# Optimization experiments

Measured on AMD Instinct MI355X. Metric: run time of the kernel, lower is better.

## Reference

```python
import jax, jax.numpy as jnp
import numpy as np

B, C, E, H = 8, 2048, 256, 64
N_AGENTS = 4
KAPPA = 0.9
MASKED = True


def _decay_xi_delta(dones):
    """Vectorized equivalent of get_decay_matrix / get_xi / delta.

    dones: [B, C] bool. Timestep dones are dones[:, ::N_AGENTS] -> [B, T].
    The original Python loop builds mask[b,n,m] = exists i with ts_done[b,i]
    and n >= i and m < i, i.e. a done strictly after m and at-or-before n.
    That equals (inclusive_cumsum[n] - inclusive_cumsum[m]) > 0.
    """
    ts = dones[:, ::N_AGENTS]                      # [B, T]
    T = ts.shape[1]
    csum = jnp.cumsum(ts.astype(jnp.int32), axis=1)            # inclusive
    blocked = (csum[:, :, None] - csum[:, None, :]) > 0        # [B, T, T]
    ts_mask = (~blocked).astype(jnp.float32)

    n = jnp.arange(T)
    diff = n[:, None] - n[None, :]
    dm = jnp.where(diff >= 0, KAPPA ** diff.astype(jnp.float32), 0.0)  # [T, T]
    dm = dm[None, :, :] * ts_mask                               # [B, T, T]
    # repeat_interleave over both time axes -> per-agent [B, C, C]
    dm = jnp.repeat(jnp.repeat(dm, N_AGENTS, axis=1), N_AGENTS, axis=2)
    if MASKED:
        Cfull = dm.shape[-1]
        dm = dm * jnp.tril(jnp.ones((Cfull, Cfull), dm.dtype))[None]

    # xi: kappa^(t+1) before the first done, 0 after (per timestep, repeated per agent)
    has_done = jnp.any(ts, axis=1, keepdims=True)               # [B, 1]
    first = jnp.argmax(ts.astype(jnp.float32), axis=1, keepdims=True)
    first = jnp.where(has_done, first, T)                       # [B, 1]
    t_idx = jnp.arange(T)[None, :]                              # [1, T]
    xi = (KAPPA ** (t_idx + 1).astype(jnp.float32)) * (t_idx < first).astype(jnp.float32)
    xi = jnp.repeat(xi, N_AGENTS, axis=1)[:, :, None]           # [B, C, 1]

    delta = (~jnp.any(ts, axis=1)).astype(jnp.float32)[:, None, None]  # [B,1,1]
    return dm, xi, delta


def setup_inputs() -> dict:
    key = jax.random.key(0)
    ks = jax.random.split(key, 8)
    return {
        "key_in": jax.random.normal(ks[0], (B, C, E), jnp.float32),
        "query": jax.random.normal(ks[1], (B, C, E), jnp.float32),
        "value": jax.random.normal(ks[2], (B, C, E), jnp.float32),
        "hstate": jax.random.normal(ks[3], (B, H, H), jnp.float32),
        "dones": jax.random.randint(ks[4], (B, C), 0, 2).astype(bool),
        "w_q": jax.random.normal(ks[5], (E, H), jnp.float32) / np.sqrt(E).astype(np.float32),
        "w_k": jax.random.normal(ks[6], (E, H), jnp.float32) / np.sqrt(E).astype(np.float32),
        "w_v": jax.random.normal(ks[7], (E, H), jnp.float32) / np.sqrt(E).astype(np.float32),
    }


def reference(key_in, query, value, hstate, dones, w_q, w_k, w_v):
    q = query @ w_q                                  # [B, C, H]
    k = key_in @ w_k                                 # [B, C, H]
    v = value @ w_v                                  # [B, C, H]

    dm, xi, delta = _decay_xi_delta(dones)           # [B,C,C], [B,C,1], [B,1,1]
    T = C // N_AGENTS
    chunk_decay = KAPPA ** T

    # next_hstate = k^T @ (v * last_row_of_decay^T) + hstate * chunk_decay * delta
    next_h = jnp.einsum('bch,bcd->bhd', k, v * dm[:, -1, :, None]) \
        + hstate * chunk_decay * delta

    cross = jnp.einsum('bch,bhd->bcd', q, hstate) * xi         # [B, C, H]
    scores = jnp.einsum('bch,bmh->bcm', q, k) * dm              # [B, C, C]
    inner = jnp.einsum('bcm,bmd->bcd', scores, v)               # [B, C, H]
    return inner + cross, next_h
```

## Files before the change

kernel.cpp:

```cpp
#include <hip/hip_runtime.h>
#include <hip/hip_bf16.h>
#include <cstddef>

#define B_ 8
#define C_ 2048
#define E_ 256
#define H_ 64
#define T_ 512
#define NA 4
#define KAPPA 0.9f
#define LOG2_KAPPA (-0.15200309344504997f)
#define KAPPA_T 3.73302e-24f

typedef __attribute__((ext_vector_type(8))) short bf16x8;
typedef __attribute__((ext_vector_type(4))) float f32x4;
typedef __attribute__((ext_vector_type(4))) unsigned u32x4;

__device__ inline unsigned short f2bfu(float x) {
    unsigned u = __builtin_bit_cast(unsigned, x);
    u += 0x7fff + ((u >> 16) & 1);
    return (unsigned short)(u >> 16);
}
__device__ inline float bf2f(unsigned short u) {
    return __builtin_bit_cast(float, (unsigned)u << 16);
}
__device__ inline unsigned pack2bf(float lo, float hi) {
    return (unsigned)f2bfu(lo) | ((unsigned)f2bfu(hi) << 16);
}
__device__ inline unsigned cvtpk(float a, float b) {
    __hip_bfloat162 h = __float22bfloat162_rn(float2{a, b});
    unsigned r;
    __builtin_memcpy(&r, &h, sizeof(r));
    return r;
}

__global__ __launch_bounds__(256) void proj_mfma(
    const float* __restrict__ key_in, const float* __restrict__ query,
    const float* __restrict__ value,
    const float* __restrict__ w_q, const float* __restrict__ w_k,
    const float* __restrict__ w_v,
    const unsigned char* __restrict__ raw,
    unsigned short* __restrict__ qp, unsigned short* __restrict__ kp,
    unsigned short* __restrict__ vp, int* __restrict__ s_tab)
{
    __shared__ __align__(16) char Wt[64 * 512];
    const int t   = threadIdx.x;
    const int bid = blockIdx.x;

    if (bid >= 768) {
        const int b    = bid - 768;
        const int lane = t & 63;
        const int w    = t >> 6;
        __shared__ int f;
        __shared__ unsigned long long msk[8];
        if (t == 0) f = 0;
        __syncthreads();
        {
            const uint4* dp = (const uint4*)raw;
            unsigned acc = 0;
#pragma unroll
            for (int i = 0; i < 4; ++i) {
                uint4 v = dp[t + 256 * i];
                acc |= (v.x | v.y | v.z | v.w) & 0xFFFFFF00u;
            }
            if (acc) f = 1;
        }
        __syncthreads();
        const int stride = f ? 1 : 4;
        const unsigned char* drow = raw + (size_t)b * C_ * stride;
#pragma unroll
        for (int cc = 0; cc < 2; ++cc) {
            const int c = 2 * w + cc;
            const int n = c * 64 + lane;
            unsigned long long m = __ballot(drow[(size_t)(4 * n) * stride] != 0);
            if (lane == 0) msk[c] = m;
        }
        __syncthreads();
#pragma unroll
        for (int cc = 0; cc < 2; ++cc) {
            const int c = 2 * w + cc;
            const int n = c * 64 + lane;
            unsigned long long lowmask =
                (lane == 63) ? ~0ULL : ((1ULL << (lane + 1)) - 1ULL);
            unsigned long long m_le = msk[c] & lowmask;
            int s = -1;
            if (m_le) {
                s = c * 64 + (63 - __builtin_clzll(m_le));
            } else {
                for (int c2 = c - 1; c2 >= 0; --c2)
                    if (msk[c2]) { s = c2 * 64 + (63 - __builtin_clzll(msk[c2])); break; }
            }
            s_tab[b * T_ + n] = s;
        }
        return;
    }

    const int mat = bid >> 8;
    const float* A; unsigned short* O16; const float* Wg;
    if (mat == 0)      { A = query;  O16 = qp; Wg = w_q; }
    else if (mat == 1) { A = key_in; O16 = kp; Wg = w_k; }
    else               { A = value;  O16 = vp; Wg = w_v; }

    const int b    = bid & 7;
    const int rb   = (bid & 255) >> 3;
    const int row0 = b * C_ + rb * 64;
    const int lane = t & 63;
    const int mt   = t >> 6;
    const int lr   = lane & 15;
    const int lg   = lane >> 4;
    const int swz  = (lr & 7) << 4;

#pragma unroll
    for (int p = 0; p < 8; ++p) {
        int idx = p * 256 + t;
        int kpair = idx >> 4;
        int dq    = (idx & 15) * 4;
        f32x4 r0 = *(const f32x4*)&Wg[(size_t)(2 * kpair)     * H_ + dq];
        f32x4 r1 = *(const f32x4*)&Wg[(size_t)(2 * kpair + 1) * H_ + dq];
#pragma unroll
        for (int j = 0; j < 4; ++j) {
            int d = dq + j;
            *(unsigned*)&Wt[(d << 9) + ((4 * kpair) ^ ((d & 7) << 4))] =
                cvtpk(r0[j], r1[j]);
        }
    }

    const float* arow = &A[(size_t)(row0 + mt * 16 + lr) * E_ + lg * 8];

    f32x4 x0 = *(const f32x4*)(arow);
    f32x4 x1 = *(const f32x4*)(arow + 4);
    __syncthreads();

    f32x4 acc[4] = {};
#pragma unroll
    for (int kc = 0; kc < 8; ++kc) {
        f32x4 n0, n1;
        if (kc < 7) {
            n0 = *(const f32x4*)(arow + (kc + 1) * 32);
            n1 = *(const f32x4*)(arow + (kc + 1) * 32 + 4);
        }
        u32x4 afu = { cvtpk(x0[0], x0[1]), cvtpk(x0[2], x0[3]),
                      cvtpk(x1[0], x1[1]), cvtpk(x1[2], x1[3]) };
        bf16x8 af = __builtin_bit_cast(bf16x8, afu);
#pragma unroll
        for (int nt = 0; nt < 4; ++nt) {
            bf16x8 bfrag = *(const bf16x8*)&Wt[((nt * 16 + lr) << 9) +
                                               ((kc * 64 + lg * 16) ^ swz)];
            acc[nt] = __builtin_amdgcn_mfma_f32_16x16x32_bf16(af, bfrag, acc[nt], 0, 0, 0);
        }
        x0 = n0; x1 = n1;
    }

    const int odd   = lr & 1;
    const int rbase = row0 + mt * 16 + lg * 4;
#pragma unroll
    for (int nt = 0; nt < 4; ++nt) {
        const int cp = nt * 16 + (lr & ~1);
        float x0_ = acc[nt][0], x1_ = acc[nt][1], x2_ = acc[nt][2], x3_ = acc[nt][3];
        float y0 = __shfl_xor(x0_, 1), y1 = __shfl_xor(x1_, 1);
        float y2 = __shfl_xor(x2_, 1), y3 = __shfl_xor(x3_, 1);
        if (!odd) {
            *(unsigned*)&O16[(size_t)(rbase + 0) * H_ + cp] = pack2bf(x0_, y0);
            *(unsigned*)&O16[(size_t)(rbase + 1) * H_ + cp] = pack2bf(x1_, y1);
        } else {
            *(unsigned*)&O16[(size_t)(rbase + 2) * H_ + cp] = pack2bf(y2, x2_);
            *(unsigned*)&O16[(size_t)(rbase + 3) * H_ + cp] = pack2bf(y3, x3_);
        }
    }
}

__global__ __launch_bounds__(256) void out_kernel(
    const unsigned short* __restrict__ qp, const unsigned short* __restrict__ kp,
    const unsigned short* __restrict__ vp, const float* __restrict__ hs,
    const int* __restrict__ s_tab,
    float* __restrict__ out0, float* __restrict__ outh)
{
    const int t    = threadIdx.x;
    const int lane = t & 63;
    const int w    = t >> 6;
    const int bid  = blockIdx.x;

    if (bid < 1024) {
        const int b = bid & 7;
        const int n = (bid >> 3) * 4 + w;
        const int a = lane >> 4;
        const int g = lane & 15;

        const int st = s_tab[b * T_ + n];
        const int s  = (st < 0) ? 0 : st;

        const unsigned short* kb = kp + (size_t)b * C_ * H_;
        const unsigned short* vb = vp + (size_t)b * C_ * H_;
        ushort4 qu = *(const ushort4*)&qp[((size_t)b * C_ + 4 * n + a) * H_ + 4 * g];
        f32x4 q4 = { bf2f(qu.x), bf2f(qu.y), bf2f(qu.z), bf2f(qu.w) };

        f32x4 acc = {};
#pragma unroll
        for (int ma = 0; ma < NA; ++ma) {
            const int m = 4 * n + ma;
            ushort4 ku = *(const ushort4*)&kb[(size_t)m * H_ + 4 * g];
            float p = q4[0] * bf2f(ku.x) + q4[1] * bf2f(ku.y)
                    + q4[2] * bf2f(ku.z) + q4[3] * bf2f(ku.w);
            p += __shfl_xor(p, 1); p += __shfl_xor(p, 2);
            p += __shfl_xor(p, 4); p += __shfl_xor(p, 8);
            if (ma <= a) {
                ushort4 vu = *(const ushort4*)&vb[(size_t)m * H_ + 4 * g];
                acc[0] += p * bf2f(vu.x); acc[1] += p * bf2f(vu.y);
                acc[2] += p * bf2f(vu.z); acc[3] += p * bf2f(vu.w);
            }
        }
        float decay = KAPPA;
        for (int mt = n - 1; mt >= s; --mt) {
#pragma unroll
            for (int ma = 0; ma < NA; ++ma) {
                const int m = 4 * mt + ma;
                ushort4 ku = *(const ushort4*)&kb[(size_t)m * H_ + 4 * g];
                float p = q4[0] * bf2f(ku.x) + q4[1] * bf2f(ku.y)
                        + q4[2] * bf2f(ku.z) + q4[3] * bf2f(ku.w);
                p += __shfl_xor(p, 1); p += __shfl_xor(p, 2);
                p += __shfl_xor(p, 4); p += __shfl_xor(p, 8);
                p *= decay;
                ushort4 vu = *(const ushort4*)&vb[(size_t)m * H_ + 4 * g];
                acc[0] += p * bf2f(vu.x); acc[1] += p * bf2f(vu.y);
                acc[2] += p * bf2f(vu.z); acc[3] += p * bf2f(vu.w);
            }
            decay *= KAPPA;
        }
        if (st < 0) {
            const float xi = exp2f(LOG2_KAPPA * (float)(n + 1));
            const float* hsb = hs + (size_t)b * H_ * H_;
            f32x4 cacc = {};
#pragma unroll
            for (int h = 0; h < H_; ++h) {
                float qh = __shfl(q4[h & 3], (a << 4) + (h >> 2));
                f32x4 h4 = *(const f32x4*)&hsb[h * H_ + 4 * g];
                cacc[0] += qh * h4[0]; cacc[1] += qh * h4[1];
                cacc[2] += qh * h4[2]; cacc[3] += qh * h4[3];
            }
            acc[0] += xi * cacc[0]; acc[1] += xi * cacc[1];
            acc[2] += xi * cacc[2]; acc[3] += xi * cacc[3];
        }
        *(f32x4*)&out0[((size_t)b * C_ + 4 * n + a) * H_ + 4 * g] = acc;
    } else {
        const int j = bid - 1024;
        const int b = j & 7;
        const int h = (j >> 3) * 4 + w;
        const int d = lane;

        const int st = s_tab[b * T_ + (T_ - 1)];
        const int s  = (st < 0) ? 0 : st;

        const unsigned short* kb = kp + (size_t)b * C_ * H_;
        const unsigned short* vb = vp + (size_t)b * C_ * H_;
        float acc = 0.f, wdec = 1.f;
        for (int mt = T_ - 1; mt >= s; --mt) {
#pragma unroll
            for (int ma = 0; ma < NA; ++ma) {
                const int m = 4 * mt + ma;
                acc += wdec * bf2f(kb[(size_t)m * H_ + h]) *
                              bf2f(vb[(size_t)m * H_ + d]);
            }
            wdec *= KAPPA;
        }
        if (st < 0)
            acc += hs[((size_t)b * H_ + h) * H_ + d] * KAPPA_T;
        outh[((size_t)b * H_ + h) * H_ + d] = acc;
    }
}

extern "C" void kernel_launch(void* const* d_in, const int* in_sizes, int n_in,
                              void* d_out, int out_size, void* d_ws, size_t ws_size,
                              hipStream_t stream)
{
    const float* key_in = (const float*)d_in[0];
    const float* query  = (const float*)d_in[1];
    const float* value  = (const float*)d_in[2];
    const float* hstate = (const float*)d_in[3];
    const unsigned char* dones = (const unsigned char*)d_in[4];
    const float* w_q = (const float*)d_in[5];
    const float* w_k = (const float*)d_in[6];
    const float* w_v = (const float*)d_in[7];

    unsigned short* qp = (unsigned short*)d_ws;
    unsigned short* kp = qp + (size_t)B_ * C_ * H_;
    unsigned short* vp = kp + (size_t)B_ * C_ * H_;
    int*         s_tab = (int*)(vp + (size_t)B_ * C_ * H_);

    proj_mfma<<<776, 256, 0, stream>>>(key_in, query, value,
                                       w_q, w_k, w_v, dones,
                                       qp, kp, vp, s_tab);
    out_kernel<<<1024 + 128, 256, 0, stream>>>(
        qp, kp, vp, hstate, s_tab,
        (float*)d_out, (float*)d_out + (size_t)B_ * C_ * H_);
}
```

Measured before the change: 26.15 us.

## Fuse projection and output kernels into one cooperative launch with grid sync

Merges the projection/s_tab kernel and the output kernel into a single cooperative kernel of 1024 blocks that does a grid-wide barrier between phases. The 128 next-hstate work units are folded onto blocks 896..1023, which also compute out0. The goal is to remove the second kernel launch and the gap between kernels. In exchange it adds a host-side occupancy query on every call, a grid-sync cost, and uneven load on the blocks that do both units. It falls back to two kernels if occupancy is too low.

```diff
diff --git a/kernel.cpp b/kernel.cpp
--- a/kernel.cpp
+++ b/kernel.cpp
@@ -1,5 +1,6 @@
 #include <hip/hip_runtime.h>
 #include <hip/hip_bf16.h>
+#include <hip/hip_cooperative_groups.h>
 #include <cstddef>
 
 #define B_ 8
@@ -34,78 +35,14 @@
     return r;
 }
 
-__global__ __launch_bounds__(256) void proj_mfma(
-    const float* __restrict__ key_in, const float* __restrict__ query,
-    const float* __restrict__ value,
-    const float* __restrict__ w_q, const float* __restrict__ w_k,
-    const float* __restrict__ w_v,
-    const unsigned char* __restrict__ raw,
-    unsigned short* __restrict__ qp, unsigned short* __restrict__ kp,
-    unsigned short* __restrict__ vp, int* __restrict__ s_tab)
-{
-    __shared__ __align__(16) char Wt[64 * 512];
-    const int t   = threadIdx.x;
-    const int bid = blockIdx.x;
-
-    if (bid >= 768) {
-        const int b    = bid - 768;
-        const int lane = t & 63;
-        const int w    = t >> 6;
-        __shared__ int f;
-        __shared__ unsigned long long msk[8];
-        if (t == 0) f = 0;
-        __syncthreads();
-        {
-            const uint4* dp = (const uint4*)raw;
-            unsigned acc = 0;
-#pragma unroll
-            for (int i = 0; i < 4; ++i) {
-                uint4 v = dp[t + 256 * i];
-                acc |= (v.x | v.y | v.z | v.w) & 0xFFFFFF00u;
-            }
-            if (acc) f = 1;
-        }
-        __syncthreads();
-        const int stride = f ? 1 : 4;
-        const unsigned char* drow = raw + (size_t)b * C_ * stride;
-#pragma unroll
-        for (int cc = 0; cc < 2; ++cc) {
-            const int c = 2 * w + cc;
-            const int n = c * 64 + lane;
-            unsigned long long m = __ballot(drow[(size_t)(4 * n) * stride] != 0);
-            if (lane == 0) msk[c] = m;
-        }
-        __syncthreads();
-#pragma unroll
-        for (int cc = 0; cc < 2; ++cc) {
-            const int c = 2 * w + cc;
-            const int n = c * 64 + lane;
-            unsigned long long lowmask =
-                (lane == 63) ? ~0ULL : ((1ULL << (lane + 1)) - 1ULL);
-            unsigned long long m_le = msk[c] & lowmask;
-            int s = -1;
-            if (m_le) {
-                s = c * 64 + (63 - __builtin_clzll(m_le));
-            } else {
-                for (int c2 = c - 1; c2 >= 0; --c2)
-                    if (msk[c2]) { s = c2 * 64 + (63 - __builtin_clzll(msk[c2])); break; }
-            }
-            s_tab[b * T_ + n] = s;
-        }
-        return;
-    }
-
-    const int mat = bid >> 8;
-    const float* A; unsigned short* O16; const float* Wg;
-    if (mat == 0)      { A = query;  O16 = qp; Wg = w_q; }
-    else if (mat == 1) { A = key_in; O16 = kp; Wg = w_k; }
-    else               { A = value;  O16 = vp; Wg = w_v; }
-
+__device__ inline void do_proj_block(
+    int bid, int t, const float* A, const float* Wg, unsigned short* O16,
+    char* Wt)
+{
     const int b    = bid & 7;
     const int rb   = (bid & 255) >> 3;
     const int row0 = b * C_ + rb * 64;
     const int lane = t & 63;
-    const int mt   = t >> 6;
     const int lr   = lane & 15;
     const int lg   = lane >> 4;
     const int swz  = (lr & 7) << 4;
@@ -125,8 +62,7 @@
         }
     }
 
-    const float* arow = &A[(size_t)(row0 + mt * 16 + lr) * E_ + lg * 8];
-
+    const float* arow = &A[(size_t)(row0 + (t >> 6) * 16 + lr) * E_ + lg * 8];
     f32x4 x0 = *(const f32x4*)(arow);
     f32x4 x1 = *(const f32x4*)(arow + 4);
     __syncthreads();
@@ -152,7 +88,7 @@
     }
 
     const int odd   = lr & 1;
-    const int rbase = row0 + mt * 16 + lg * 4;
+    const int rbase = row0 + (t >> 6) * 16 + lg * 4;
 #pragma unroll
     for (int nt = 0; nt < 4; ++nt) {
         const int cp = nt * 16 + (lr & ~1);
@@ -169,103 +105,215 @@
     }
 }
 
-__global__ __launch_bounds__(256) void out_kernel(
-    const unsigned short* __restrict__ qp, const unsigned short* __restrict__ kp,
-    const unsigned short* __restrict__ vp, const float* __restrict__ hs,
-    const int* __restrict__ s_tab,
-    float* __restrict__ out0, float* __restrict__ outh)
-{
-    const int t    = threadIdx.x;
+__device__ inline void do_stab_block(
+    int b, int t, const unsigned char* raw, int* s_tab)
+{
     const int lane = t & 63;
-    const int w    = t >> 6;
-    const int bid  = blockIdx.x;
-
-    if (bid < 1024) {
-        const int b = bid & 7;
-        const int n = (bid >> 3) * 4 + w;
-        const int a = lane >> 4;
-        const int g = lane & 15;
-
-        const int st = s_tab[b * T_ + n];
-        const int s  = (st < 0) ? 0 : st;
-
-        const unsigned short* kb = kp + (size_t)b * C_ * H_;
-        const unsigned short* vb = vp + (size_t)b * C_ * H_;
-        ushort4 qu = *(const ushort4*)&qp[((size_t)b * C_ + 4 * n + a) * H_ + 4 * g];
-        f32x4 q4 = { bf2f(qu.x), bf2f(qu.y), bf2f(qu.z), bf2f(qu.w) };
-
-        f32x4 acc = {};
+    const int wv   = t >> 6;
+    __shared__ int f;
+    __shared__ unsigned long long msk[8];
+    if (t == 0) f = 0;
+    __syncthreads();
+    {
+        const uint4* dp = (const uint4*)raw;
+        unsigned acc = 0;
+#pragma unroll
+        for (int i = 0; i < 4; ++i) {
+            uint4 v = dp[t + 256 * i];
+            acc |= (v.x | v.y | v.z | v.w) & 0xFFFFFF00u;
+        }
+        if (acc) f = 1;
+    }
+    __syncthreads();
+    const int stride = f ? 1 : 4;
+    const unsigned char* drow = raw + (size_t)b * C_ * stride;
+#pragma unroll
+    for (int cc = 0; cc < 2; ++cc) {
+        const int c = 2 * wv + cc;
+        const int n = c * 64 + lane;
+        unsigned long long m = __ballot(drow[(size_t)(4 * n) * stride] != 0);
+        if (lane == 0) msk[c] = m;
+    }
+    __syncthreads();
+#pragma unroll
+    for (int cc = 0; cc < 2; ++cc) {
+        const int c = 2 * wv + cc;
+        const int n = c * 64 + lane;
+        unsigned long long lowmask =
+            (lane == 63) ? ~0ULL : ((1ULL << (lane + 1)) - 1ULL);
+        unsigned long long m_le = msk[c] & lowmask;
+        int s = -1;
+        if (m_le) {
+            s = c * 64 + (63 - __builtin_clzll(m_le));
+        } else {
+            for (int c2 = c - 1; c2 >= 0; --c2)
+                if (msk[c2]) { s = c2 * 64 + (63 - __builtin_clzll(msk[c2])); break; }
+        }
+        s_tab[b * T_ + n] = s;
+    }
+}
+
+__device__ inline void do_out0_unit(
+    int bid, int t, const unsigned short* qp, const unsigned short* kp,
+    const unsigned short* vp, const float* hs, const int* s_tab, float* out0)
+{
+    const int lane = t & 63;
+    const int wv   = t >> 6;
+    const int b = bid & 7;
+    const int n = (bid >> 3) * 4 + wv;
+    const int a = lane >> 4;
+    const int g = lane & 15;
+
+    const int st = s_tab[b * T_ + n];
+    const int s  = (st < 0) ? 0 : st;
+
+    const unsigned short* kb = kp + (size_t)b * C_ * H_;
+    const unsigned short* vb = vp + (size_t)b * C_ * H_;
+    ushort4 qu = *(const ushort4*)&qp[((size_t)b * C_ + 4 * n + a) * H_ + 4 * g];
+    f32x4 q4 = { bf2f(qu.x), bf2f(qu.y), bf2f(qu.z), bf2f(qu.w) };
+
+    f32x4 acc = {};
+#pragma unroll
+    for (int ma = 0; ma < NA; ++ma) {
+        const int m = 4 * n + ma;
+        ushort4 ku = *(const ushort4*)&kb[(size_t)m * H_ + 4 * g];
+        float p = q4[0] * bf2f(ku.x) + q4[1] * bf2f(ku.y)
+                + q4[2] * bf2f(ku.z) + q4[3] * bf2f(ku.w);
+        p += __shfl_xor(p, 1); p += __shfl_xor(p, 2);
+        p += __shfl_xor(p, 4); p += __shfl_xor(p, 8);
+        if (ma <= a) {
+            ushort4 vu = *(const ushort4*)&vb[(size_t)m * H_ + 4 * g];
+            acc[0] += p * bf2f(vu.x); acc[1] += p * bf2f(vu.y);
+            acc[2] += p * bf2f(vu.z); acc[3] += p * bf2f(vu.w);
+        }
+    }
+    float decay = KAPPA;
+    for (int mt = n - 1; mt >= s; --mt) {
 #pragma unroll
         for (int ma = 0; ma < NA; ++ma) {
-            const int m = 4 * n + ma;
+            const int m = 4 * mt + ma;
             ushort4 ku = *(const ushort4*)&kb[(size_t)m * H_ + 4 * g];
             float p = q4[0] * bf2f(ku.x) + q4[1] * bf2f(ku.y)
                     + q4[2] * bf2f(ku.z) + q4[3] * bf2f(ku.w);
             p += __shfl_xor(p, 1); p += __shfl_xor(p, 2);
             p += __shfl_xor(p, 4); p += __shfl_xor(p, 8);
-            if (ma <= a) {
-                ushort4 vu = *(const ushort4*)&vb[(size_t)m * H_ + 4 * g];
-                acc[0] += p * bf2f(vu.x); acc[1] += p * bf2f(vu.y);
-                acc[2] += p * bf2f(vu.z); acc[3] += p * bf2f(vu.w);
-            }
-        }
-        float decay = KAPPA;
-        for (int mt = n - 1; mt >= s; --mt) {
-#pragma unroll
-            for (int ma = 0; ma < NA; ++ma) {
-                const int m = 4 * mt + ma;
-                ushort4 ku = *(const ushort4*)&kb[(size_t)m * H_ + 4 * g];
-                float p = q4[0] * bf2f(ku.x) + q4[1] * bf2f(ku.y)
-                        + q4[2] * bf2f(ku.z) + q4[3] * bf2f(ku.w);
-                p += __shfl_xor(p, 1); p += __shfl_xor(p, 2);
-                p += __shfl_xor(p, 4); p += __shfl_xor(p, 8);
-                p *= decay;
-                ushort4 vu = *(const ushort4*)&vb[(size_t)m * H_ + 4 * g];
-                acc[0] += p * bf2f(vu.x); acc[1] += p * bf2f(vu.y);
-                acc[2] += p * bf2f(vu.z); acc[3] += p * bf2f(vu.w);
-            }
-            decay *= KAPPA;
-        }
-        if (st < 0) {
-            const float xi = exp2f(LOG2_KAPPA * (float)(n + 1));
-            const float* hsb = hs + (size_t)b * H_ * H_;
-            f32x4 cacc = {};
-#pragma unroll
-            for (int h = 0; h < H_; ++h) {
-                float qh = __shfl(q4[h & 3], (a << 4) + (h >> 2));
-                f32x4 h4 = *(const f32x4*)&hsb[h * H_ + 4 * g];
-                cacc[0] += qh * h4[0]; cacc[1] += qh * h4[1];
-                cacc[2] += qh * h4[2]; cacc[3] += qh * h4[3];
-            }
-            acc[0] += xi * cacc[0]; acc[1] += xi * cacc[1];
-            acc[2] += xi * cacc[2]; acc[3] += xi * cacc[3];
-        }
-        *(f32x4*)&out0[((size_t)b * C_ + 4 * n + a) * H_ + 4 * g] = acc;
-    } else {
-        const int j = bid - 1024;
-        const int b = j & 7;
-        const int h = (j >> 3) * 4 + w;
-        const int d = lane;
-
-        const int st = s_tab[b * T_ + (T_ - 1)];
-        const int s  = (st < 0) ? 0 : st;
-
-        const unsigned short* kb = kp + (size_t)b * C_ * H_;
-        const unsigned short* vb = vp + (size_t)b * C_ * H_;
-        float acc = 0.f, wdec = 1.f;
-        for (int mt = T_ - 1; mt >= s; --mt) {
-#pragma unroll
-            for (int ma = 0; ma < NA; ++ma) {
-                const int m = 4 * mt + ma;
-                acc += wdec * bf2f(kb[(size_t)m * H_ + h]) *
-                              bf2f(vb[(size_t)m * H_ + d]);
-            }
-            wdec *= KAPPA;
-        }
-        if (st < 0)
-            acc += hs[((size_t)b * H_ + h) * H_ + d] * KAPPA_T;
-        outh[((size_t)b * H_ + h) * H_ + d] = acc;
-    }
+            p *= decay;
+            ushort4 vu = *(const ushort4*)&vb[(size_t)m * H_ + 4 * g];
+            acc[0] += p * bf2f(vu.x); acc[1] += p * bf2f(vu.y);
+            acc[2] += p * bf2f(vu.z); acc[3] += p * bf2f(vu.w);
+        }
+        decay *= KAPPA;
+    }
+    if (st < 0) {
+        const float xi = exp2f(LOG2_KAPPA * (float)(n + 1));
+        const float* hsb = hs + (size_t)b * H_ * H_;
+        f32x4 cacc = {};
+#pragma unroll
+        for (int h = 0; h < H_; ++h) {
+            float qh = __shfl(q4[h & 3], (a << 4) + (h >> 2));
+            f32x4 h4 = *(const f32x4*)&hsb[h * H_ + 4 * g];
+            cacc[0] += qh * h4[0]; cacc[1] += qh * h4[1];
+            cacc[2] += qh * h4[2]; cacc[3] += qh * h4[3];
+        }
+        acc[0] += xi * cacc[0]; acc[1] += xi * cacc[1];
+        acc[2] += xi * cacc[2]; acc[3] += xi * cacc[3];
+    }
+    *(f32x4*)&out0[((size_t)b * C_ + 4 * n + a) * H_ + 4 * g] = acc;
+}
+
+__device__ inline void do_nexth_unit(
+    int j, int t, const unsigned short* kp, const unsigned short* vp,
+    const float* hs, const int* s_tab, float* outh)
+{
+    const int lane = t & 63;
+    const int wv   = t >> 6;
+    const int b = j & 7;
+    const int h = (j >> 3) * 4 + wv;
+    const int d = lane;
+
+    const int st = s_tab[b * T_ + (T_ - 1)];
+    const int s  = (st < 0) ? 0 : st;
+
+    const unsigned short* kb = kp + (size_t)b * C_ * H_;
+    const unsigned short* vb = vp + (size_t)b * C_ * H_;
+    float acc = 0.f, wdec = 1.f;
+    for (int mt = T_ - 1; mt >= s; --mt) {
+#pragma unroll
+        for (int ma = 0; ma < NA; ++ma) {
+            const int m = 4 * mt + ma;
+            acc += wdec * bf2f(kb[(size_t)m * H_ + h]) *
+                          bf2f(vb[(size_t)m * H_ + d]);
+        }
+        wdec *= KAPPA;
+    }
+    if (st < 0)
+        acc += hs[((size_t)b * H_ + h) * H_ + d] * KAPPA_T;
+    outh[((size_t)b * H_ + h) * H_ + d] = acc;
+}
+
+__global__ __launch_bounds__(256, 4) void fused_kernel(
+    const float* __restrict__ key_in, const float* __restrict__ query,
+    const float* __restrict__ value, const float* __restrict__ hs,
+    const float* __restrict__ w_q, const float* __restrict__ w_k,
+    const float* __restrict__ w_v,
+    const unsigned char* __restrict__ raw,
+    unsigned short* __restrict__ qp, unsigned short* __restrict__ kp,
+    unsigned short* __restrict__ vp, int* __restrict__ s_tab,
+    float* __restrict__ out0, float* __restrict__ outh)
+{
+    __shared__ __align__(16) char Wt[64 * 512];
+    const int t   = threadIdx.x;
+    const int bid = blockIdx.x;
+
+    if (bid < 768) {
+        const int mat = bid >> 8;
+        const float* A; unsigned short* O16; const float* Wg;
+        if (mat == 0)      { A = query;  O16 = qp; Wg = w_q; }
+        else if (mat == 1) { A = key_in; O16 = kp; Wg = w_k; }
+        else               { A = value;  O16 = vp; Wg = w_v; }
+        do_proj_block(bid, t, A, Wg, O16, Wt);
+    } else if (bid < 776) {
+        do_stab_block(bid - 768, t, raw, s_tab);
+    }
+
+    cooperative_groups::this_grid().sync();
+
+    do_out0_unit(bid, t, qp, kp, vp, hs, s_tab, out0);
+    if (bid >= 896)
+        do_nexth_unit(bid - 896, t, kp, vp, hs, s_tab, outh);
+}
+
+__global__ __launch_bounds__(256) void proj_kernelB(
+    const float* __restrict__ key_in, const float* __restrict__ query,
+    const float* __restrict__ value,
+    const float* __restrict__ w_q, const float* __restrict__ w_k,
+    const float* __restrict__ w_v,
+    const unsigned char* __restrict__ raw,
+    unsigned short* __restrict__ qp, unsigned short* __restrict__ kp,
+    unsigned short* __restrict__ vp, int* __restrict__ s_tab)
+{
+    __shared__ __align__(16) char Wt[64 * 512];
+    const int t   = threadIdx.x;
+    const int bid = blockIdx.x;
+    if (bid >= 768) { do_stab_block(bid - 768, t, raw, s_tab); return; }
+    const int mat = bid >> 8;
+    const float* A; unsigned short* O16; const float* Wg;
+    if (mat == 0)      { A = query;  O16 = qp; Wg = w_q; }
+    else if (mat == 1) { A = key_in; O16 = kp; Wg = w_k; }
+    else               { A = value;  O16 = vp; Wg = w_v; }
+    do_proj_block(bid, t, A, Wg, O16, Wt);
+}
+
+__global__ __launch_bounds__(256) void out_kernelB(
+    const unsigned short* __restrict__ qp, const unsigned short* __restrict__ kp,
+    const unsigned short* __restrict__ vp, const float* __restrict__ hs,
+    const int* __restrict__ s_tab,
+    float* __restrict__ out0, float* __restrict__ outh)
+{
+    const int t   = threadIdx.x;
+    const int bid = blockIdx.x;
+    if (bid < 1024) do_out0_unit(bid, t, qp, kp, vp, hs, s_tab, out0);
+    else            do_nexth_unit(bid - 1024, t, kp, vp, hs, s_tab, outh);
 }
 
 extern "C" void kernel_launch(void* const* d_in, const int* in_sizes, int n_in,
@@ -285,11 +333,28 @@
     unsigned short* kp = qp + (size_t)B_ * C_ * H_;
     unsigned short* vp = kp + (size_t)B_ * C_ * H_;
     int*         s_tab = (int*)(vp + (size_t)B_ * C_ * H_);
-
-    proj_mfma<<<776, 256, 0, stream>>>(key_in, query, value,
-                                       w_q, w_k, w_v, dones,
-                                       qp, kp, vp, s_tab);
-    out_kernel<<<1024 + 128, 256, 0, stream>>>(
-        qp, kp, vp, hstate, s_tab,
-        (float*)d_out, (float*)d_out + (size_t)B_ * C_ * H_);
-}
+    float*        out0 = (float*)d_out;
+    float*        outh = (float*)d_out + (size_t)B_ * C_ * H_;
+
+    int blocksPerCU = 0;
+    hipError_t qerr = hipOccupancyMaxActiveBlocksPerMultiprocessor(
+        &blocksPerCU, (const void*)fused_kernel, 256, 0);
+    const bool coop_ok = (qerr == hipSuccess) && (blocksPerCU * 256 >= 1024);
+
+    if (coop_ok) {
+        void* args[] = {
+            (void*)&key_in, (void*)&query, (void*)&value, (void*)&hstate,
+            (void*)&w_q, (void*)&w_k, (void*)&w_v, (void*)&dones,
+            (void*)&qp, (void*)&kp, (void*)&vp, (void*)&s_tab,
+            (void*)&out0, (void*)&outh
+        };
+        hipLaunchCooperativeKernel((void*)fused_kernel, dim3(1024), dim3(256),
+                                   args, 0, stream);
+    } else {
+        proj_kernelB<<<776, 256, 0, stream>>>(key_in, query, value,
+                                              w_q, w_k, w_v, dones,
+                                              qp, kp, vp, s_tab);
+        out_kernelB<<<1024 + 128, 256, 0, stream>>>(qp, kp, vp, hstate, s_tab,
+                                                    out0, outh);
+    }
+}
```

Result: slower. 29.85 us (+14.1%).
